# Kernel tuning notes

Measured on AMD Instinct MI355X. Metric: run time of the kernel, lower is better.

The kernel has to match this reference:

```python
import jax, jax.numpy as jnp
import numpy as np

NUM_HEADS = 16
MASK_VALUE = -10000.0


def setup_inputs() -> dict:
    key = jax.random.key(0)
    ks = jax.random.split(key, 5)
    B, S, D = 2, 2048, 1024
    std = 0.02
    return {
        "hidden_states": jax.random.normal(ks[0], (B, S, D), dtype=jnp.float32),
        "wq": jax.random.normal(ks[1], (D, D), dtype=jnp.float32) * std,
        "bq": jnp.zeros((D,), dtype=jnp.float32),
        "wk": jax.random.normal(ks[2], (D, D), dtype=jnp.float32) * std,
        "bk": jnp.zeros((D,), dtype=jnp.float32),
        "wv": jax.random.normal(ks[3], (D, D), dtype=jnp.float32) * std,
        "bv": jnp.zeros((D,), dtype=jnp.float32),
        "wc": jax.random.normal(ks[4], (D, D), dtype=jnp.float32) * std,
        "bc": jnp.zeros((D,), dtype=jnp.float32),
    }


def reference(hidden_states, wq, bq, wk, bk, wv, bv, wc, bc):
    B, S, D = hidden_states.shape
    H = NUM_HEADS
    hd = D // H

    def split_heads(x):  # [B,S,D] -> [B,H,S,hd]
        return x.reshape(B, S, H, hd).transpose(0, 2, 1, 3)

    q = split_heads(hidden_states @ wq + bq)
    k = split_heads(hidden_states @ wk + bk)
    v = split_heads(hidden_states @ wv + bv)

    # eager QK^T with scale_attn_weights (divide by sqrt(head_dim))
    attn_weights = jnp.einsum("bhqd,bhkd->bhqk", q, k) / jnp.sqrt(
        jnp.asarray(hd, dtype=q.dtype))

    # causal mask (attention_mask is None, not cross-attention)
    causal = jnp.tril(jnp.ones((S, S), dtype=bool))[None, None]
    attn_weights = jnp.where(causal, attn_weights,
                             jnp.asarray(MASK_VALUE, dtype=attn_weights.dtype))

    attn_weights = jax.nn.softmax(attn_weights, axis=-1)
    # attn_dropout p=0.0 (eval) -> identity; no head_mask

    attn_output = jnp.einsum("bhqk,bhkd->bhqd", attn_weights, v)
    attn_output = attn_output.transpose(0, 2, 1, 3).reshape(B, S, D)
    attn_output = attn_output @ wc + bc  # c_proj; resid_dropout p=0 -> identity
    return attn_output, attn_weights, k, v
```

## Files before the change

### kernel.cpp

```cpp
#include <hip/hip_runtime.h>


typedef __attribute__((ext_vector_type(8))) short bf8_t;
typedef __attribute__((ext_vector_type(4))) float f4_t;

#define MFMA(a, b, c) __builtin_amdgcn_mfma_f32_16x16x32_bf16(a, b, c, 0, 0, 0)

static __device__ __forceinline__ unsigned short f2bf(float f) {
    union { float f; unsigned u; } x; x.f = f;
    unsigned u = x.u;
    return (unsigned short)((u + 0x7fffu + ((u >> 16) & 1u)) >> 16);
}

static __device__ __forceinline__ void stage16(const unsigned short* g, unsigned short* lbase) {
    __builtin_amdgcn_global_load_lds(
        (const __attribute__((address_space(1))) unsigned int*)g,
        (__attribute__((address_space(3))) unsigned int*)lbase, 16, 0, 0);
}

#define NE 4194304ULL
#define AW 134217728ULL


__global__ void cast_hidden(const float* __restrict__ src, unsigned short* __restrict__ dst) {
    int i = (blockIdx.x * 256 + threadIdx.x) * 4;
    float4 h = *(const float4*)(src + i);
    ushort4 o;
    o.x = f2bf(h.x); o.y = f2bf(h.y); o.z = f2bf(h.z); o.w = f2bf(h.w);
    *(ushort4*)(dst + i) = o;
}

__global__ void transpose_w(const float* __restrict__ wq, const float* __restrict__ wk,
                            const float* __restrict__ wv, const float* __restrict__ wc,
                            unsigned short* __restrict__ wqkvT, unsigned short* __restrict__ wcT) {
    __shared__ float tile[32][33];
    int z = blockIdx.z;
    const float* W = z == 0 ? wq : z == 1 ? wk : z == 2 ? wv : wc;
    unsigned short* dst = (z < 3) ? (wqkvT + (size_t)z * 1024 * 1024) : wcT;
    int x0 = blockIdx.x * 32, y0 = blockIdx.y * 32;
    int tx = threadIdx.x, ty = threadIdx.y;
#pragma unroll
    for (int i = 0; i < 4; ++i)
        tile[ty + i * 8][tx] = W[(size_t)(y0 + ty + i * 8) * 1024 + x0 + tx];
    __syncthreads();
#pragma unroll
    for (int i = 0; i < 4; ++i)
        dst[(size_t)(x0 + ty + i * 8) * 1024 + y0 + tx] = f2bf(tile[tx][ty + i * 8]);
}


#define GEMM_CORE(A_, B_, KDIM)                                                             \
    const int m0 = blockIdx.y * 128, n0 = blockIdx.x * 128;                                 \
    const int tid = threadIdx.x, w = tid >> 6, lane = tid & 63, ln = lane & 15,             \
              quad = lane >> 4;                                                             \
    const int wm = (w & 1) * 64, wn = (w >> 1) * 64;                                        \
    f4_t acc[4][4] = {};                                                                    \
    for (int kb = 0; kb < (KDIM); kb += 64) {                                               \
        __syncthreads();                                                                    \
        _Pragma("unroll")                                                                   \
        for (int p = 0; p < 4; ++p) {                                                       \
            int t = (w * 4 + p) * 64 + lane;                                                \
            int r = t >> 3, c = (t & 7) ^ (r & 7);                                          \
            stage16(&(A_)[(size_t)(m0 + r) * (KDIM) + kb + c * 8], &As[(w * 4 + p) * 512]); \
            stage16(&(B_)[(size_t)(n0 + r) * (KDIM) + kb + c * 8], &Bs[(w * 4 + p) * 512]); \
        }                                                                                   \
        __syncthreads();                                                                    \
        bf8_t af[2][4], bfm[2][4];                                                          \
        _Pragma("unroll")                                                                   \
        for (int h = 0; h < 2; ++h) {                                                       \
            _Pragma("unroll")                                                               \
            for (int i = 0; i < 4; ++i) {                                                   \
                int c = (h * 4 + quad) ^ (ln & 7);                                          \
                af[h][i] = *(const bf8_t*)&As[(wm + i * 16 + ln) * 64 + c * 8];             \
                bfm[h][i] = *(const bf8_t*)&Bs[(wn + i * 16 + ln) * 64 + c * 8];            \
            }                                                                               \
        }                                                                                   \
        _Pragma("unroll")                                                                   \
        for (int h = 0; h < 2; ++h)                                                         \
            _Pragma("unroll")                                                               \
            for (int i = 0; i < 4; ++i)                                                     \
                _Pragma("unroll")                                                           \
                for (int j = 0; j < 4; ++j)                                                 \
                    acc[i][j] = MFMA(af[h][i], bfm[h][j], acc[i][j]);                       \
    }

__global__ __launch_bounds__(256) void gemm_qkv(
    const unsigned short* __restrict__ A, const unsigned short* __restrict__ BT,
    const float* __restrict__ bq, const float* __restrict__ bk, const float* __restrict__ bv,
    unsigned short* __restrict__ q_bf, unsigned short* __restrict__ k_bf,
    unsigned short* __restrict__ vT_bf, float* __restrict__ out_k, float* __restrict__ out_v)
{
    __shared__ __align__(16) unsigned short As[128 * 64];
    __shared__ __align__(16) unsigned short Bs[128 * 64];
    GEMM_CORE(A, BT, 1024)
#pragma unroll
    for (int j = 0; j < 4; ++j) {
        int coln = n0 + wn + j * 16 + ln;
        int which = coln >> 10, d = coln & 1023, h = d >> 6, e = d & 63;
        float bias = which == 0 ? bq[d] : (which == 1 ? bk[d] : bv[d]);
#pragma unroll
        for (int i = 0; i < 4; ++i) {
#pragma unroll
            for (int v = 0; v < 4; ++v) {
                int row = m0 + wm + i * 16 + quad * 4 + v;
                int b = row >> 11, s = row & 2047;
                float val = acc[i][j][v] + bias;
                size_t hidx = (((size_t)(b * 16 + h)) * 2048 + s) * 64 + e;
                if (which == 0) {
                    q_bf[hidx] = f2bf(val * 0.125f);
                } else if (which == 1) {
                    k_bf[hidx] = f2bf(val);
                    out_k[hidx] = val;
                } else {
                    vT_bf[((size_t)(b * 16 + h) * 64 + e) * 2048 + s] = f2bf(val);
                    out_v[hidx] = val;
                }
            }
        }
    }
}

__global__ __launch_bounds__(256) void gemm_cproj(
    const unsigned short* __restrict__ A, const unsigned short* __restrict__ BT,
    const float* __restrict__ bc, float* __restrict__ out)
{
    __shared__ __align__(16) unsigned short As[128 * 64];
    __shared__ __align__(16) unsigned short Bs[128 * 64];
    GEMM_CORE(A, BT, 1024)
#pragma unroll
    for (int j = 0; j < 4; ++j) {
        int coln = n0 + wn + j * 16 + ln;
        float bias = bc[coln];
#pragma unroll
        for (int i = 0; i < 4; ++i) {
#pragma unroll
            for (int v = 0; v < 4; ++v) {
                int row = m0 + wm + i * 16 + quad * 4 + v;
                out[(size_t)row * 1024 + coln] = acc[i][j][v] + bias;
            }
        }
    }
}

__global__ __launch_bounds__(256) void attn_fused(
    const unsigned short* __restrict__ q_bf,
    const unsigned short* __restrict__ k_bf,
    const unsigned short* __restrict__ vT_bf,
    float* __restrict__ attn_w,
    unsigned short* __restrict__ attnpre)
{
    __shared__ __align__(16) unsigned short Qlds[128 * 72];
    __shared__ __align__(16) float Pf32[4][16 * 36];
    const int bh = blockIdx.x;
    const int q0 = (15 - blockIdx.y) * 128;
    const int tid = threadIdx.x, w = tid >> 6, lane = tid & 63, ln = lane & 15, quad = lane >> 4;
#pragma unroll
    for (int p = 0; p < 4; ++p) {
        int c = tid + p * 256;
        int r = c >> 3, e0 = (c & 7) * 8;
        *(uint4*)&Qlds[r * 72 + e0] = *(const uint4*)&q_bf[((size_t)bh * 2048 + q0 + r) * 64 + e0];
    }
    __syncthreads();
    const int s0 = w * 16, s1 = 64 + w * 16;
    const int g0 = q0 + s0, g1 = q0 + s1;
    const int rmax0 = g0 + 15, rmax1 = g1 + 15;
    bf8_t aA0 = *(const bf8_t*)&Qlds[(s0 + ln) * 72 + quad * 8];
    bf8_t aA1 = *(const bf8_t*)&Qlds[(s0 + ln) * 72 + 32 + quad * 8];
    bf8_t aB0 = *(const bf8_t*)&Qlds[(s1 + ln) * 72 + quad * 8];
    bf8_t aB1 = *(const bf8_t*)&Qlds[(s1 + ln) * 72 + 32 + quad * 8];
    const unsigned short* kb_base = k_bf + (size_t)bh * 2048 * 64;

    f4_t l0v = {0.f, 0.f, 0.f, 0.f}, l1v = {0.f, 0.f, 0.f, 0.f};
    const f4_t zf = {0.f, 0.f, 0.f, 0.f};
    const int nkt = (rmax1 >> 4) + 1;
    for (int kt = 0; kt < nkt; ++kt) {
        int col0 = kt * 16, col = col0 + ln;
        const unsigned short* kp = kb_base + (size_t)(col0 + ln) * 64 + quad * 8;
        bf8_t b0 = *(const bf8_t*)kp;
        bf8_t b1 = *(const bf8_t*)(kp + 32);
        f4_t sc = MFMA(aB0, b0, zf); sc = MFMA(aB1, b1, sc);
#pragma unroll
        for (int v = 0; v < 4; ++v) {
            if (col <= g1 + quad * 4 + v) l1v[v] += __expf(sc[v]);
        }
        if (col0 <= rmax0) {
            f4_t sc0 = MFMA(aA0, b0, zf); sc0 = MFMA(aA1, b1, sc0);
#pragma unroll
            for (int v = 0; v < 4; ++v) {
                if (col <= g0 + quad * 4 + v) l0v[v] += __expf(sc0[v]);
            }
        }
    }
#pragma unroll
    for (int m = 1; m < 16; m <<= 1) {
#pragma unroll
        for (int v = 0; v < 4; ++v) {
            l0v[v] += __shfl_xor(l0v[v], m);
            l1v[v] += __shfl_xor(l1v[v], m);
        }
    }
    f4_t linv0, linv1;
#pragma unroll
    for (int v = 0; v < 4; ++v) { linv0[v] = 1.f / l0v[v]; linv1[v] = 1.f / l1v[v]; }

    f4_t o0[4] = {}, o1[4] = {};
    float* awp = attn_w + (size_t)bh * 2048 * 2048;
    const unsigned short* vt_base = vT_bf + (size_t)bh * 64 * 2048;
    float* pw = &Pf32[w][0];
    for (int kc = 0; kc < 64; ++kc) {
        int col0c = kc * 32;
        bool act1 = col0c <= rmax1, act0 = col0c <= rmax0;
        bf8_t kf[4], vb[4];
        if (act1) {
#pragma unroll
            for (int sub = 0; sub < 2; ++sub) {
                const unsigned short* kp = kb_base + (size_t)(col0c + sub * 16 + ln) * 64 + quad * 8;
                kf[sub * 2] = *(const bf8_t*)kp;
                kf[sub * 2 + 1] = *(const bf8_t*)(kp + 32);
            }
#pragma unroll
            for (int j = 0; j < 4; ++j)
                vb[j] = *(const bf8_t*)(vt_base + (size_t)(j * 16 + ln) * 2048 + col0c + quad * 8);
        }
        auto do_strip = [&](int gb, bf8_t a0, bf8_t a1, const f4_t& linv, f4_t* oacc, bool active) {
            if (active) {
#pragma unroll
                for (int sub = 0; sub < 2; ++sub) {
                    f4_t sc = MFMA(a0, kf[sub * 2], zf);
                    sc = MFMA(a1, kf[sub * 2 + 1], sc);
                    int col = col0c + sub * 16 + ln;
#pragma unroll
                    for (int v = 0; v < 4; ++v) {
                        int row = gb + quad * 4 + v;
                        float p = (col <= row) ? __expf(sc[v]) * linv[v] : 0.f;
                        pw[(quad * 4 + v) * 36 + sub * 16 + ln] = p;
                    }
                }
#pragma unroll
                for (int half = 0; half < 2; ++half) {
                    int r = half * 8 + (lane >> 3), cq = lane & 7;
                    float4 val = *(const float4*)&pw[r * 36 + cq * 4];
                    *(float4*)&awp[(size_t)(gb + r) * 2048 + col0c + cq * 4] = val;
                }
                float4 pa = *(const float4*)&pw[ln * 36 + quad * 8];
                float4 pb = *(const float4*)&pw[ln * 36 + quad * 8 + 4];
                bf8_t pf;
                pf[0] = (short)f2bf(pa.x); pf[1] = (short)f2bf(pa.y);
                pf[2] = (short)f2bf(pa.z); pf[3] = (short)f2bf(pa.w);
                pf[4] = (short)f2bf(pb.x); pf[5] = (short)f2bf(pb.y);
                pf[6] = (short)f2bf(pb.z); pf[7] = (short)f2bf(pb.w);
#pragma unroll
                for (int j = 0; j < 4; ++j) oacc[j] = MFMA(pf, vb[j], oacc[j]);
            } else {
                float4 z4 = {0.f, 0.f, 0.f, 0.f};
#pragma unroll
                for (int half = 0; half < 2; ++half) {
                    int r = half * 8 + (lane >> 3), cq = lane & 7;
                    *(float4*)&awp[(size_t)(gb + r) * 2048 + col0c + cq * 4] = z4;
                }
            }
        };
        do_strip(g1, aB0, aB1, linv1, o1, act1);
        do_strip(g0, aA0, aA1, linv0, o0, act0);
    }
    int b = bh >> 4, h = bh & 15;
#pragma unroll
    for (int j = 0; j < 4; ++j) {
#pragma unroll
        for (int v = 0; v < 4; ++v) {
            int e = h * 64 + j * 16 + ln;
            attnpre[(size_t)(b * 2048 + g0 + quad * 4 + v) * 1024 + e] = f2bf(o0[j][v]);
            attnpre[(size_t)(b * 2048 + g1 + quad * 4 + v) * 1024 + e] = f2bf(o1[j][v]);
        }
    }
}

extern "C" void kernel_launch(void* const* d_in, const int* in_sizes, int n_in,
                              void* d_out, int out_size, void* d_ws, size_t ws_size,
                              hipStream_t stream)
{
    const float* hs = (const float*)d_in[0];
    const float* wq = (const float*)d_in[1];
    const float* bq = (const float*)d_in[2];
    const float* wk = (const float*)d_in[3];
    const float* bk = (const float*)d_in[4];
    const float* wv = (const float*)d_in[5];
    const float* bv = (const float*)d_in[6];
    const float* wc = (const float*)d_in[7];
    const float* bc = (const float*)d_in[8];

    float* out      = (float*)d_out;
    float* out_aw   = out + NE;
    float* out_k    = out_aw + AW;
    float* out_v    = out_k + NE;

    char* ws = (char*)d_ws;
    unsigned short* hid_bf  = (unsigned short*)(ws);
    unsigned short* wqkvT   = (unsigned short*)(ws + 8388608);
    unsigned short* wcT     = (unsigned short*)(ws + 14680064);
    unsigned short* q_bf    = (unsigned short*)(ws + 16777216);
    unsigned short* k_bf    = (unsigned short*)(ws + 25165824);
    unsigned short* vT_bf   = (unsigned short*)(ws + 33554432);
    unsigned short* attnpre = (unsigned short*)(ws + 41943040);

    cast_hidden<<<4096, 256, 0, stream>>>(hs, hid_bf);
    transpose_w<<<dim3(32, 32, 4), dim3(32, 8), 0, stream>>>(wq, wk, wv, wc, wqkvT, wcT);
    gemm_qkv<<<dim3(24, 32), 256, 0, stream>>>(hid_bf, wqkvT, bq, bk, bv,
                                               q_bf, k_bf, vT_bf, out_k, out_v);
    attn_fused<<<dim3(32, 16), 256, 0, stream>>>(q_bf, k_bf, vT_bf, out_aw, attnpre);
    gemm_cproj<<<dim3(8, 32), 256, 0, stream>>>(attnpre, wcT, bc, out);
}
```

Measured before the change: 814.4 us.

## Split attention blocks to 64 query rows and use nontemporal stores for outputs

The attention kernel now gives each block 64 query rows with one 16-row strip per wave, not 128 rows with two strips, and launches twice as many blocks. Q fragments are read straight from global memory, which drops the LDS staging and the barrier. Masked upper-triangle columns are zeroed in a separate tail loop. Large fp32 outputs (attention weights, k, v, c_proj output) are written with nontemporal stores to reduce cache pollution. The smaller blocks improve load balance and occupancy, but K/V reuse across strips within a block is lost, so each K/V tile is read by more blocks.

```diff
diff --git a/kernel.cpp b/kernel.cpp
--- a/kernel.cpp
+++ b/kernel.cpp
@@ -110,10 +110,10 @@
                     q_bf[hidx] = f2bf(val * 0.125f);
                 } else if (which == 1) {
                     k_bf[hidx] = f2bf(val);
-                    out_k[hidx] = val;
+                    __builtin_nontemporal_store(val, &out_k[hidx]);
                 } else {
                     vT_bf[((size_t)(b * 16 + h) * 64 + e) * 2048 + s] = f2bf(val);
-                    out_v[hidx] = val;
+                    __builtin_nontemporal_store(val, &out_v[hidx]);
                 }
             }
         }
@@ -136,7 +136,7 @@
 #pragma unroll
             for (int v = 0; v < 4; ++v) {
                 int row = m0 + wm + i * 16 + quad * 4 + v;
-                out[(size_t)row * 1024 + coln] = acc[i][j][v] + bias;
+                __builtin_nontemporal_store(acc[i][j][v] + bias, &out[(size_t)row * 1024 + coln]);
             }
         }
     }
@@ -149,119 +149,95 @@
     float* __restrict__ attn_w,
     unsigned short* __restrict__ attnpre)
 {
-    __shared__ __align__(16) unsigned short Qlds[128 * 72];
     __shared__ __align__(16) float Pf32[4][16 * 36];
     const int bh = blockIdx.x;
-    const int q0 = (15 - blockIdx.y) * 128;
+    const int q0 = (31 - blockIdx.y) * 64;
     const int tid = threadIdx.x, w = tid >> 6, lane = tid & 63, ln = lane & 15, quad = lane >> 4;
-#pragma unroll
-    for (int p = 0; p < 4; ++p) {
-        int c = tid + p * 256;
-        int r = c >> 3, e0 = (c & 7) * 8;
-        *(uint4*)&Qlds[r * 72 + e0] = *(const uint4*)&q_bf[((size_t)bh * 2048 + q0 + r) * 64 + e0];
-    }
-    __syncthreads();
-    const int s0 = w * 16, s1 = 64 + w * 16;
-    const int g0 = q0 + s0, g1 = q0 + s1;
-    const int rmax0 = g0 + 15, rmax1 = g1 + 15;
-    bf8_t aA0 = *(const bf8_t*)&Qlds[(s0 + ln) * 72 + quad * 8];
-    bf8_t aA1 = *(const bf8_t*)&Qlds[(s0 + ln) * 72 + 32 + quad * 8];
-    bf8_t aB0 = *(const bf8_t*)&Qlds[(s1 + ln) * 72 + quad * 8];
-    bf8_t aB1 = *(const bf8_t*)&Qlds[(s1 + ln) * 72 + 32 + quad * 8];
+    const int g0 = q0 + w * 16;
+    const int rmax = g0 + 15;
+    const unsigned short* qb = q_bf + ((size_t)bh * 2048 + g0) * 64;
+    bf8_t aA0 = *(const bf8_t*)&qb[(size_t)ln * 64 + quad * 8];
+    bf8_t aA1 = *(const bf8_t*)&qb[(size_t)ln * 64 + 32 + quad * 8];
     const unsigned short* kb_base = k_bf + (size_t)bh * 2048 * 64;
-
-    f4_t l0v = {0.f, 0.f, 0.f, 0.f}, l1v = {0.f, 0.f, 0.f, 0.f};
     const f4_t zf = {0.f, 0.f, 0.f, 0.f};
-    const int nkt = (rmax1 >> 4) + 1;
+
+    f4_t lv = {0.f, 0.f, 0.f, 0.f};
+    const int nkt = (rmax >> 4) + 1;
     for (int kt = 0; kt < nkt; ++kt) {
-        int col0 = kt * 16, col = col0 + ln;
-        const unsigned short* kp = kb_base + (size_t)(col0 + ln) * 64 + quad * 8;
+        int col = kt * 16 + ln;
+        const unsigned short* kp = kb_base + (size_t)col * 64 + quad * 8;
         bf8_t b0 = *(const bf8_t*)kp;
         bf8_t b1 = *(const bf8_t*)(kp + 32);
-        f4_t sc = MFMA(aB0, b0, zf); sc = MFMA(aB1, b1, sc);
+        f4_t sc = MFMA(aA0, b0, zf); sc = MFMA(aA1, b1, sc);
 #pragma unroll
         for (int v = 0; v < 4; ++v) {
-            if (col <= g1 + quad * 4 + v) l1v[v] += __expf(sc[v]);
-        }
-        if (col0 <= rmax0) {
-            f4_t sc0 = MFMA(aA0, b0, zf); sc0 = MFMA(aA1, b1, sc0);
-#pragma unroll
-            for (int v = 0; v < 4; ++v) {
-                if (col <= g0 + quad * 4 + v) l0v[v] += __expf(sc0[v]);
-            }
+            if (col <= g0 + quad * 4 + v) lv[v] += __expf(sc[v]);
         }
     }
 #pragma unroll
     for (int m = 1; m < 16; m <<= 1) {
 #pragma unroll
-        for (int v = 0; v < 4; ++v) {
-            l0v[v] += __shfl_xor(l0v[v], m);
-            l1v[v] += __shfl_xor(l1v[v], m);
-        }
-    }
-    f4_t linv0, linv1;
-#pragma unroll
-    for (int v = 0; v < 4; ++v) { linv0[v] = 1.f / l0v[v]; linv1[v] = 1.f / l1v[v]; }
-
-    f4_t o0[4] = {}, o1[4] = {};
+        for (int v = 0; v < 4; ++v) lv[v] += __shfl_xor(lv[v], m);
+    }
+    f4_t linv;
+#pragma unroll
+    for (int v = 0; v < 4; ++v) linv[v] = 1.f / lv[v];
+
+    f4_t o[4] = {};
     float* awp = attn_w + (size_t)bh * 2048 * 2048;
     const unsigned short* vt_base = vT_bf + (size_t)bh * 64 * 2048;
     float* pw = &Pf32[w][0];
-    for (int kc = 0; kc < 64; ++kc) {
+    const int nact = (rmax >> 5) + 1;
+    for (int kc = 0; kc < nact; ++kc) {
         int col0c = kc * 32;
-        bool act1 = col0c <= rmax1, act0 = col0c <= rmax0;
         bf8_t kf[4], vb[4];
-        if (act1) {
-#pragma unroll
-            for (int sub = 0; sub < 2; ++sub) {
-                const unsigned short* kp = kb_base + (size_t)(col0c + sub * 16 + ln) * 64 + quad * 8;
-                kf[sub * 2] = *(const bf8_t*)kp;
-                kf[sub * 2 + 1] = *(const bf8_t*)(kp + 32);
+#pragma unroll
+        for (int sub = 0; sub < 2; ++sub) {
+            const unsigned short* kp = kb_base + (size_t)(col0c + sub * 16 + ln) * 64 + quad * 8;
+            kf[sub * 2] = *(const bf8_t*)kp;
+            kf[sub * 2 + 1] = *(const bf8_t*)(kp + 32);
+        }
+#pragma unroll
+        for (int j = 0; j < 4; ++j)
+            vb[j] = *(const bf8_t*)(vt_base + (size_t)(j * 16 + ln) * 2048 + col0c + quad * 8);
+#pragma unroll
+        for (int sub = 0; sub < 2; ++sub) {
+            f4_t sc = MFMA(aA0, kf[sub * 2], zf);
+            sc = MFMA(aA1, kf[sub * 2 + 1], sc);
+            int col = col0c + sub * 16 + ln;
+#pragma unroll
+            for (int v = 0; v < 4; ++v) {
+                int row = g0 + quad * 4 + v;
+                float p = (col <= row) ? __expf(sc[v]) * linv[v] : 0.f;
+                pw[(quad * 4 + v) * 36 + sub * 16 + ln] = p;
             }
-#pragma unroll
-            for (int j = 0; j < 4; ++j)
-                vb[j] = *(const bf8_t*)(vt_base + (size_t)(j * 16 + ln) * 2048 + col0c + quad * 8);
-        }
-        auto do_strip = [&](int gb, bf8_t a0, bf8_t a1, const f4_t& linv, f4_t* oacc, bool active) {
-            if (active) {
-#pragma unroll
-                for (int sub = 0; sub < 2; ++sub) {
-                    f4_t sc = MFMA(a0, kf[sub * 2], zf);
-                    sc = MFMA(a1, kf[sub * 2 + 1], sc);
-                    int col = col0c + sub * 16 + ln;
-#pragma unroll
-                    for (int v = 0; v < 4; ++v) {
-                        int row = gb + quad * 4 + v;
-                        float p = (col <= row) ? __expf(sc[v]) * linv[v] : 0.f;
-                        pw[(quad * 4 + v) * 36 + sub * 16 + ln] = p;
-                    }
-                }
-#pragma unroll
-                for (int half = 0; half < 2; ++half) {
-                    int r = half * 8 + (lane >> 3), cq = lane & 7;
-                    float4 val = *(const float4*)&pw[r * 36 + cq * 4];
-                    *(float4*)&awp[(size_t)(gb + r) * 2048 + col0c + cq * 4] = val;
-                }
-                float4 pa = *(const float4*)&pw[ln * 36 + quad * 8];
-                float4 pb = *(const float4*)&pw[ln * 36 + quad * 8 + 4];
-                bf8_t pf;
-                pf[0] = (short)f2bf(pa.x); pf[1] = (short)f2bf(pa.y);
-                pf[2] = (short)f2bf(pa.z); pf[3] = (short)f2bf(pa.w);
-                pf[4] = (short)f2bf(pb.x); pf[5] = (short)f2bf(pb.y);
-                pf[6] = (short)f2bf(pb.z); pf[7] = (short)f2bf(pb.w);
-#pragma unroll
-                for (int j = 0; j < 4; ++j) oacc[j] = MFMA(pf, vb[j], oacc[j]);
-            } else {
-                float4 z4 = {0.f, 0.f, 0.f, 0.f};
-#pragma unroll
-                for (int half = 0; half < 2; ++half) {
-                    int r = half * 8 + (lane >> 3), cq = lane & 7;
-                    *(float4*)&awp[(size_t)(gb + r) * 2048 + col0c + cq * 4] = z4;
-                }
-            }
-        };
-        do_strip(g1, aB0, aB1, linv1, o1, act1);
-        do_strip(g0, aA0, aA1, linv0, o0, act0);
+        }
+#pragma unroll
+        for (int half = 0; half < 2; ++half) {
+            int r = half * 8 + (lane >> 3), cq = lane & 7;
+            f4_t val = *(const f4_t*)&pw[r * 36 + cq * 4];
+            __builtin_nontemporal_store(val, (f4_t*)&awp[(size_t)(g0 + r) * 2048 + col0c + cq * 4]);
+        }
+        f4_t pa = *(const f4_t*)&pw[ln * 36 + quad * 8];
+        f4_t pb = *(const f4_t*)&pw[ln * 36 + quad * 8 + 4];
+        bf8_t pf;
+        pf[0] = (short)f2bf(pa[0]); pf[1] = (short)f2bf(pa[1]);
+        pf[2] = (short)f2bf(pa[2]); pf[3] = (short)f2bf(pa[3]);
+        pf[4] = (short)f2bf(pb[0]); pf[5] = (short)f2bf(pb[1]);
+        pf[6] = (short)f2bf(pb[2]); pf[7] = (short)f2bf(pb[3]);
+#pragma unroll
+        for (int j = 0; j < 4; ++j) o[j] = MFMA(pf, vb[j], o[j]);
+    }
+    {
+        const f4_t z4 = {0.f, 0.f, 0.f, 0.f};
+        int r = (lane >> 3), cq = lane & 7;
+        float* aw0 = awp + (size_t)(g0 + r) * 2048 + cq * 4;
+        for (int kc = nact; kc < 64; ++kc) {
+            int col0c = kc * 32;
+#pragma unroll
+            for (int half = 0; half < 2; ++half)
+                __builtin_nontemporal_store(z4, (f4_t*)(aw0 + (size_t)half * 8 * 2048 + col0c));
+        }
     }
     int b = bh >> 4, h = bh & 15;
 #pragma unroll
@@ -269,8 +245,7 @@
 #pragma unroll
         for (int v = 0; v < 4; ++v) {
             int e = h * 64 + j * 16 + ln;
-            attnpre[(size_t)(b * 2048 + g0 + quad * 4 + v) * 1024 + e] = f2bf(o0[j][v]);
-            attnpre[(size_t)(b * 2048 + g1 + quad * 4 + v) * 1024 + e] = f2bf(o1[j][v]);
+            attnpre[(size_t)(b * 2048 + g0 + quad * 4 + v) * 1024 + e] = f2bf(o[j][v]);
         }
     }
 }
@@ -307,6 +282,6 @@
     transpose_w<<<dim3(32, 32, 4), dim3(32, 8), 0, stream>>>(wq, wk, wv, wc, wqkvT, wcT);
     gemm_qkv<<<dim3(24, 32), 256, 0, stream>>>(hid_bf, wqkvT, bq, bk, bv,
                                                q_bf, k_bf, vT_bf, out_k, out_v);
-    attn_fused<<<dim3(32, 16), 256, 0, stream>>>(q_bf, k_bf, vT_bf, out_aw, attnpre);
+    attn_fused<<<dim3(32, 32), 256, 0, stream>>>(q_bf, k_bf, vT_bf, out_aw, attnpre);
     gemm_cproj<<<dim3(8, 32), 256, 0, stream>>>(attnpre, wcT, bc, out);
 }
```

After: 808.7 us. No clear change (-0.7%).
